# Optimization experiments

Hardware: AMD Instinct MI355X
Metric: run time of the kernel (lower is better)

The kernel has to match this reference:

```python
import jax, jax.numpy as jnp
import numpy as np

N, D_IN, D_HID, D_OUT, ORDER = 8192, 512, 1024, 64, 3

def setup_inputs() -> dict:
    key = jax.random.key(0)
    k = jax.random.split(key, 5)
    x = jax.random.normal(k[0], (N, D_IN), dtype=jnp.float32)
    adj = jax.random.uniform(k[1], (ORDER, N, N), dtype=jnp.float32)
    W1 = jax.random.normal(k[2], (ORDER, D_IN, D_HID), dtype=jnp.float32) * (1.0 / np.sqrt(D_IN))
    b1 = jnp.zeros((D_HID,), dtype=jnp.float32)
    W2 = jax.random.normal(k[3], (ORDER, D_HID, D_OUT), dtype=jnp.float32) * (1.0 / np.sqrt(D_HID))
    b2 = jnp.zeros((D_OUT,), dtype=jnp.float32)
    return {"x": x, "preprocessed": adj, "W1": W1, "b1": b1, "W2": W2, "b2": b2}

def multi_val_gc(x, adj, W, b):
    # x: [N, in], adj: [order, N, N], W: [order, in, out]
    xw = jnp.einsum('ni,kio->kno', x, W)          # [order, N, out]
    out = jnp.einsum('knm,kmo->no', adj, xw)      # sum over orders
    return out + b

def reference(x, preprocessed, W1, b1, W2, b2):
    h = multi_val_gc(x, preprocessed, W1, b1)
    h = jax.nn.relu(h)
    # dropout is identity in eval mode
    h = multi_val_gc(h, preprocessed, W2, b2)
    return jax.nn.log_softmax(h, axis=1)
```

## Files before the change

### kernel.cpp

```cpp
#include <hip/hip_runtime.h>
#include <hip/hip_bf16.h>
#include <cstdint>
#include <cstddef>


typedef __bf16 bf16_t;
typedef __bf16 bf16x8 __attribute__((ext_vector_type(8)));
typedef __bf16 bf16x4 __attribute__((ext_vector_type(4)));
typedef float  f32x4  __attribute__((ext_vector_type(4)));

#define NROWS 8192
#define DIN   512
#define DHID  1024
#define DOUT  64
#define ORD   3
#define KTOT  24576

#define GLDS(g, l) __builtin_amdgcn_global_load_lds( \
    (__attribute__((address_space(1))) void*)(g),    \
    (__attribute__((address_space(3))) void*)(l), 16, 0, 0)


__global__ void k_cvt_x(const float* __restrict__ x, bf16_t* __restrict__ xb) {
  int i = blockIdx.x * blockDim.x + threadIdx.x;
  const float4* p = reinterpret_cast<const float4*>(x) + (size_t)i * 2;
  float4 v0 = p[0], v1 = p[1];
  bf16x8 o;
  o[0]=(bf16_t)v0.x; o[1]=(bf16_t)v0.y; o[2]=(bf16_t)v0.z; o[3]=(bf16_t)v0.w;
  o[4]=(bf16_t)v1.x; o[5]=(bf16_t)v1.y; o[6]=(bf16_t)v1.z; o[7]=(bf16_t)v1.w;
  *reinterpret_cast<bf16x8*>(xb + (size_t)i * 8) = o;
}

__global__ void k_cvt_adj(const float* __restrict__ a, bf16_t* __restrict__ ab) {
  size_t i = (size_t)blockIdx.x * blockDim.x + threadIdx.x;
  const size_t stride = (size_t)gridDim.x * blockDim.x;
  const float4* src = reinterpret_cast<const float4*>(a);
#pragma unroll 4
  for (int it = 0; it < 48; ++it, i += stride) {
    float4 v0 = src[i * 2], v1 = src[i * 2 + 1];
    bf16x8 o;
    o[0]=(bf16_t)v0.x; o[1]=(bf16_t)v0.y; o[2]=(bf16_t)v0.z; o[3]=(bf16_t)v0.w;
    o[4]=(bf16_t)v1.x; o[5]=(bf16_t)v1.y; o[6]=(bf16_t)v1.z; o[7]=(bf16_t)v1.w;
    *reinterpret_cast<bf16x8*>(ab + i * 8) = o;
  }
}

__global__ void k_transpose_cvt(const float* __restrict__ src, bf16_t* __restrict__ dst,
                                int R, int C) {
  __shared__ float tile[64][65];
  int ord = blockIdx.z;
  src += (size_t)ord * R * C;
  dst += (size_t)ord * R * C;
  int c0 = blockIdx.x * 64, r0 = blockIdx.y * 64;
  for (int i = 0; i < 16; ++i) {
    int idx = i * 256 + threadIdx.x;
    int r = idx >> 6, c = idx & 63;
    tile[r][c] = src[(size_t)(r0 + r) * C + c0 + c];
  }
  __syncthreads();
  for (int i = 0; i < 16; ++i) {
    int idx = i * 256 + threadIdx.x;
    int cc = idx >> 6, rr = idx & 63;
    dst[(size_t)(c0 + cc) * R + r0 + rr] = (bf16_t)tile[rr][cc];
  }
}

__global__ __launch_bounds__(256) void k_gemm_xw1(
    const bf16_t* __restrict__ xb,
    const bf16_t* __restrict__ w1t,
    bf16_t* __restrict__ xw1t)
{
  __shared__ bf16_t As[128 * 64];
  __shared__ bf16_t Bs[128 * 64];
  int ntile = blockIdx.x, mtile = blockIdx.y, ord = blockIdx.z;
  int tid = threadIdx.x, lane = tid & 63, wid = tid >> 6;
  int wm = wid >> 1, wn = wid & 1;
  int sl = (lane & 7) ^ (lane >> 3);
  f32x4 acc[4][4] = {};
  const bf16_t* w1o = w1t + (size_t)ord * DHID * DIN;
  for (int kt = 0; kt < DIN; kt += 64) {
    for (int j = 0; j < 4; ++j) {
      int q = wid * 4 + j;
      int row = q * 8 + (lane >> 3);
      GLDS(xb + (size_t)(mtile * 128 + row) * DIN + kt + sl * 8, &As[q * 512]);
    }
    for (int j = 0; j < 4; ++j) {
      int q = wid * 4 + j;
      int row = q * 8 + (lane >> 3);
      GLDS(w1o + (size_t)(ntile * 128 + row) * DIN + kt + sl * 8, &Bs[q * 512]);
    }
    __syncthreads();
    for (int ks = 0; ks < 2; ++ks) {
      int psl = ((ks << 2) + (lane >> 4)) ^ (lane & 7);
      bf16x8 a[4], b[4];
      for (int f = 0; f < 4; ++f)
        a[f] = *reinterpret_cast<const bf16x8*>(&As[(wm * 64 + f * 16 + (lane & 15)) * 64 + psl * 8]);
      for (int f = 0; f < 4; ++f)
        b[f] = *reinterpret_cast<const bf16x8*>(&Bs[(wn * 64 + f * 16 + (lane & 15)) * 64 + psl * 8]);
      for (int fm = 0; fm < 4; ++fm)
        for (int fn = 0; fn < 4; ++fn)
          acc[fm][fn] = __builtin_amdgcn_mfma_f32_16x16x32_bf16(a[fm], b[fn], acc[fm][fn], 0, 0, 0);
    }
    __syncthreads();
  }
  for (int fm = 0; fm < 4; ++fm)
    for (int fn = 0; fn < 4; ++fn) {
      int o  = ntile * 128 + wn * 64 + fn * 16 + (lane & 15);
      int n0 = mtile * 128 + wm * 64 + fm * 16 + ((lane >> 4) << 2);
      bf16x4 v;
      v[0] = (bf16_t)acc[fm][fn][0]; v[1] = (bf16_t)acc[fm][fn][1];
      v[2] = (bf16_t)acc[fm][fn][2]; v[3] = (bf16_t)acc[fm][fn][3];
      *reinterpret_cast<bf16x4*>(&xw1t[(size_t)o * KTOT + ord * NROWS + n0]) = v;
    }
}

__global__ __launch_bounds__(512) void k_gemm_h256(
    const bf16_t* __restrict__ adjb,
    const bf16_t* __restrict__ xw1t,
    float* __restrict__ hpart)
{
  __shared__ bf16_t As[256 * 64];
  __shared__ bf16_t Bs[256 * 64];
  int d = blockIdx.x;
  int xcd = d & 7;
  int s = d >> 3;
  int ksp = xcd & 1;
  int mtile = (xcd >> 1) * 8 + (s >> 2);
  int ntile = s & 3;
  int tid = threadIdx.x, lane = tid & 63, wid = tid >> 6;
  int wm = wid >> 2, wn = wid & 3;
  int sl = (lane & 7) ^ (lane >> 3);
  const size_t NN = (size_t)NROWS * NROWS;
  f32x4 acc[8][4] = {};
  const int T0 = ksp * 192, NT = 192;

  for (int t = 0; t < NT; ++t) {
    int kk = (T0 + t) * 64;
    int ord = kk >> 13, mcol = kk & 8191;
    const bf16_t* ao = adjb + (size_t)ord * NN + (size_t)(mtile * 256) * NROWS + mcol;
#pragma unroll
    for (int j = 0; j < 4; ++j) {
      int q = wid * 4 + j;
      int row = q * 8 + (lane >> 3);
      GLDS(ao + (size_t)row * NROWS + sl * 8, &As[q * 512]);
    }
#pragma unroll
    for (int j = 0; j < 4; ++j) {
      int q = wid * 4 + j;
      int row = q * 8 + (lane >> 3);
      GLDS(xw1t + (size_t)(ntile * 256 + row) * KTOT + kk + sl * 8, &Bs[q * 512]);
    }
    __syncthreads();
#pragma unroll
    for (int ks = 0; ks < 2; ++ks) {
      int psl = ((ks << 2) + (lane >> 4)) ^ (lane & 7);
      bf16x8 a[8], b[4];
#pragma unroll
      for (int f = 0; f < 8; ++f)
        a[f] = *reinterpret_cast<const bf16x8*>(&As[(wm * 128 + f * 16 + (lane & 15)) * 64 + psl * 8]);
#pragma unroll
      for (int f = 0; f < 4; ++f)
        b[f] = *reinterpret_cast<const bf16x8*>(&Bs[(wn * 64 + f * 16 + (lane & 15)) * 64 + psl * 8]);
#pragma unroll
      for (int fm = 0; fm < 8; ++fm)
#pragma unroll
        for (int fn = 0; fn < 4; ++fn)
          acc[fm][fn] = __builtin_amdgcn_mfma_f32_16x16x32_bf16(a[fm], b[fn], acc[fm][fn], 0, 0, 0);
    }
    __syncthreads();
  }

  float* pout = hpart + (size_t)ksp * NROWS * DHID;
#pragma unroll
  for (int fm = 0; fm < 8; ++fm)
#pragma unroll
    for (int fn = 0; fn < 4; ++fn) {
      int o  = ntile * 256 + wn * 64 + fn * 16 + (lane & 15);
      int n0 = mtile * 256 + wm * 128 + fm * 16 + ((lane >> 4) << 2);
      for (int j = 0; j < 4; ++j)
        pout[(size_t)(n0 + j) * DHID + o] = acc[fm][fn][j];
    }
}

__global__ void k_reduce_h(const float* __restrict__ hpart, const float* __restrict__ b1,
                           bf16_t* __restrict__ h) {
  size_t i4 = (size_t)blockIdx.x * blockDim.x + threadIdx.x;
  size_t base = i4 * 4;
  int col = (int)(base & (DHID - 1));
  const size_t S = (size_t)NROWS * DHID;
  float4 p0 = *reinterpret_cast<const float4*>(hpart + base);
  float4 p1 = *reinterpret_cast<const float4*>(hpart + S + base);
  float4 bb = *reinterpret_cast<const float4*>(b1 + col);
  bf16x4 v;
  float t0 = p0.x + p1.x + bb.x; v[0] = (bf16_t)(t0 > 0.f ? t0 : 0.f);
  float t1 = p0.y + p1.y + bb.y; v[1] = (bf16_t)(t1 > 0.f ? t1 : 0.f);
  float t2 = p0.z + p1.z + bb.z; v[2] = (bf16_t)(t2 > 0.f ? t2 : 0.f);
  float t3 = p0.w + p1.w + bb.w; v[3] = (bf16_t)(t3 > 0.f ? t3 : 0.f);
  *reinterpret_cast<bf16x4*>(h + base) = v;
}

__global__ __launch_bounds__(256) void k_gemm_h128(
    const bf16_t* __restrict__ adjb, const bf16_t* __restrict__ xw1t,
    const float* __restrict__ b1, bf16_t* __restrict__ h)
{
  __shared__ bf16_t As[2][128 * 64];
  __shared__ bf16_t Bs[2][128 * 64];
  int d = blockIdx.x;
  int xcd = d & 7;
  int idx = d >> 3;
  int mtile = xcd * 8 + (idx >> 3);
  int ntile = idx & 7;
  int tid = threadIdx.x, lane = tid & 63, wid = tid >> 6;
  int wm = wid >> 1, wn = wid & 1;
  int sl = (lane & 7) ^ (lane >> 3);
  const size_t NN = (size_t)NROWS * NROWS;
  f32x4 acc[4][4] = {};
  const int NT = KTOT / 64;

  auto stage = [&](int buf, int kt) {
    int kk = kt * 64;
    int ord = kk >> 13, mcol = kk & 8191;
    const bf16_t* ao = adjb + (size_t)ord * NN + (size_t)(mtile * 128) * NROWS + mcol;
#pragma unroll
    for (int jj = 0; jj < 4; ++jj) {
      int q = wid * 4 + jj;
      int row = q * 8 + (lane >> 3);
      GLDS(ao + (size_t)row * NROWS + sl * 8, &As[buf][q * 512]);
    }
#pragma unroll
    for (int jj = 0; jj < 4; ++jj) {
      int q = wid * 4 + jj;
      int row = q * 8 + (lane >> 3);
      GLDS(xw1t + (size_t)(ntile * 128 + row) * KTOT + kk + sl * 8, &Bs[buf][q * 512]);
    }
  };
  auto compute = [&](int cur) {
    const bf16_t* Ac = &As[cur][0];
    const bf16_t* Bc = &Bs[cur][0];
#pragma unroll
    for (int ks = 0; ks < 2; ++ks) {
      int psl = ((ks << 2) + (lane >> 4)) ^ (lane & 7);
      bf16x8 a[4], b[4];
      for (int f = 0; f < 4; ++f)
        a[f] = *reinterpret_cast<const bf16x8*>(&Ac[(wm * 64 + f * 16 + (lane & 15)) * 64 + psl * 8]);
      for (int f = 0; f < 4; ++f)
        b[f] = *reinterpret_cast<const bf16x8*>(&Bc[(wn * 64 + f * 16 + (lane & 15)) * 64 + psl * 8]);
      for (int fm = 0; fm < 4; ++fm)
        for (int fn = 0; fn < 4; ++fn)
          acc[fm][fn] = __builtin_amdgcn_mfma_f32_16x16x32_bf16(a[fm], b[fn], acc[fm][fn], 0, 0, 0);
    }
  };

  stage(0, 0);
  for (int t = 0; t < NT - 1; ++t) {
    int cur = t & 1;
    stage(cur ^ 1, t + 1);
    asm volatile("s_waitcnt vmcnt(8)" ::: "memory");
    __builtin_amdgcn_s_barrier();
    compute(cur);
    asm volatile("" ::: "memory");
    __builtin_amdgcn_s_barrier();
  }
  asm volatile("s_waitcnt vmcnt(0)" ::: "memory");
  __builtin_amdgcn_s_barrier();
  compute((NT - 1) & 1);

  for (int fm = 0; fm < 4; ++fm)
    for (int fn = 0; fn < 4; ++fn) {
      int o  = ntile * 128 + wn * 64 + fn * 16 + (lane & 15);
      float bias = b1[o];
      int n0 = mtile * 128 + wm * 64 + fm * 16 + ((lane >> 4) << 2);
      for (int jj = 0; jj < 4; ++jj) {
        float v = acc[fm][fn][jj] + bias;
        v = v > 0.0f ? v : 0.0f;
        h[(size_t)(n0 + jj) * DHID + o] = (bf16_t)v;
      }
    }
}

__global__ __launch_bounds__(256) void k_gemm_xw2(
    const bf16_t* __restrict__ h,
    const bf16_t* __restrict__ w2t,
    bf16_t* __restrict__ xw2t)
{
  __shared__ bf16_t As[128 * 64];
  __shared__ bf16_t Bs[64 * 64];
  int mtile = blockIdx.x, ord = blockIdx.y;
  int tid = threadIdx.x, lane = tid & 63, wid = tid >> 6;
  int wm = wid >> 1, wn = wid & 1;
  int sl = (lane & 7) ^ (lane >> 3);
  f32x4 acc[4][2] = {};
  const bf16_t* w2o = w2t + (size_t)ord * DOUT * DHID;
  for (int kt = 0; kt < DHID; kt += 64) {
    for (int j = 0; j < 4; ++j) {
      int q = wid * 4 + j;
      int row = q * 8 + (lane >> 3);
      GLDS(h + (size_t)(mtile * 128 + row) * DHID + kt + sl * 8, &As[q * 512]);
    }
    for (int j = 0; j < 2; ++j) {
      int q = wid * 2 + j;
      int row = q * 8 + (lane >> 3);
      GLDS(w2o + (size_t)row * DHID + kt + sl * 8, &Bs[q * 512]);
    }
    __syncthreads();
    for (int ks = 0; ks < 2; ++ks) {
      int psl = ((ks << 2) + (lane >> 4)) ^ (lane & 7);
      bf16x8 a[4], b[2];
      for (int f = 0; f < 4; ++f)
        a[f] = *reinterpret_cast<const bf16x8*>(&As[(wm * 64 + f * 16 + (lane & 15)) * 64 + psl * 8]);
      for (int f = 0; f < 2; ++f)
        b[f] = *reinterpret_cast<const bf16x8*>(&Bs[(wn * 32 + f * 16 + (lane & 15)) * 64 + psl * 8]);
      for (int fm = 0; fm < 4; ++fm)
        for (int fn = 0; fn < 2; ++fn)
          acc[fm][fn] = __builtin_amdgcn_mfma_f32_16x16x32_bf16(a[fm], b[fn], acc[fm][fn], 0, 0, 0);
    }
    __syncthreads();
  }
  for (int fm = 0; fm < 4; ++fm)
    for (int fn = 0; fn < 2; ++fn) {
      int o2 = wn * 32 + fn * 16 + (lane & 15);
      int n0 = mtile * 128 + wm * 64 + fm * 16 + ((lane >> 4) << 2);
      bf16x4 v;
      v[0] = (bf16_t)acc[fm][fn][0]; v[1] = (bf16_t)acc[fm][fn][1];
      v[2] = (bf16_t)acc[fm][fn][2]; v[3] = (bf16_t)acc[fm][fn][3];
      *reinterpret_cast<bf16x4*>(&xw2t[(size_t)o2 * KTOT + ord * NROWS + n0]) = v;
    }
}

__global__ __launch_bounds__(256) void k_gemm_out(
    const bf16_t* __restrict__ adjb,
    const bf16_t* __restrict__ xw2t,
    float* __restrict__ part)
{
  __shared__ bf16_t As[128 * 64];
  __shared__ bf16_t Bs[64 * 64];
  int mtile = blockIdx.x, ksp = blockIdx.y;
  int tid = threadIdx.x, lane = tid & 63, wid = tid >> 6;
  int wm = wid >> 1, wn = wid & 1;
  int sl = (lane & 7) ^ (lane >> 3);
  const size_t NN = (size_t)NROWS * NROWS;
  f32x4 acc[4][2] = {};
  for (int kt = ksp * 24; kt < ksp * 24 + 24; ++kt) {
    int kk = kt * 64;
    int ord = kk >> 13, mcol = kk & 8191;
    const bf16_t* ao = adjb + (size_t)ord * NN + (size_t)(mtile * 128) * NROWS + mcol;
    for (int j = 0; j < 4; ++j) {
      int q = wid * 4 + j;
      int row = q * 8 + (lane >> 3);
      GLDS(ao + (size_t)row * NROWS + sl * 8, &As[q * 512]);
    }
    for (int j = 0; j < 2; ++j) {
      int q = wid * 2 + j;
      int row = q * 8 + (lane >> 3);
      GLDS(xw2t + (size_t)row * KTOT + kk + sl * 8, &Bs[q * 512]);
    }
    __syncthreads();
    for (int ks = 0; ks < 2; ++ks) {
      int psl = ((ks << 2) + (lane >> 4)) ^ (lane & 7);
      bf16x8 a[4], b[2];
      for (int f = 0; f < 4; ++f)
        a[f] = *reinterpret_cast<const bf16x8*>(&As[(wm * 64 + f * 16 + (lane & 15)) * 64 + psl * 8]);
      for (int f = 0; f < 2; ++f)
        b[f] = *reinterpret_cast<const bf16x8*>(&Bs[(wn * 32 + f * 16 + (lane & 15)) * 64 + psl * 8]);
      for (int fm = 0; fm < 4; ++fm)
        for (int fn = 0; fn < 2; ++fn)
          acc[fm][fn] = __builtin_amdgcn_mfma_f32_16x16x32_bf16(a[fm], b[fn], acc[fm][fn], 0, 0, 0);
    }
    __syncthreads();
  }
  float* pout = part + (size_t)ksp * NROWS * DOUT;
  for (int fm = 0; fm < 4; ++fm)
    for (int fn = 0; fn < 2; ++fn) {
      int o2 = wn * 32 + fn * 16 + (lane & 15);
      int n0 = mtile * 128 + wm * 64 + fm * 16 + ((lane >> 4) << 2);
      for (int j = 0; j < 4; ++j)
        pout[(size_t)(n0 + j) * DOUT + o2] = acc[fm][fn][j];
    }
}

__global__ void k_logsoftmax(const float* __restrict__ part, const float* __restrict__ b2,
                             float* __restrict__ out) {
  int wid = threadIdx.x >> 6, lane = threadIdx.x & 63;
  int n = blockIdx.x * 4 + wid;
  size_t s = (size_t)NROWS * DOUT;
  float v = b2[lane];
#pragma unroll
  for (int p = 0; p < 16; ++p)
    v += part[(size_t)p * s + (size_t)n * DOUT + lane];
  float mx = v;
  for (int d = 32; d; d >>= 1) mx = fmaxf(mx, __shfl_xor(mx, d));
  float e = expf(v - mx);
  float sum = e;
  for (int d = 32; d; d >>= 1) sum += __shfl_xor(sum, d);
  out[(size_t)n * DOUT + lane] = (v - mx) - logf(sum);
}

__global__ __launch_bounds__(256) void k_gemm_h_f32(
    const float* __restrict__ adj, const bf16_t* __restrict__ xw1t,
    const float* __restrict__ b1, bf16_t* __restrict__ h)
{
  __shared__ bf16_t As[128 * 64];
  __shared__ bf16_t Bs[128 * 64];
  int d = blockIdx.x;
  int xcd = d & 7, idx = d >> 3;
  int mtile = xcd * 8 + (idx >> 3), ntile = idx & 7;
  int tid = threadIdx.x, lane = tid & 63, wid = tid >> 6;
  int wm = wid >> 1, wn = wid & 1;
  int sl = (lane & 7) ^ (lane >> 3);
  f32x4 acc[4][4] = {};
  for (int kt = 0; kt < KTOT / 64; ++kt) {
    int kk0 = kt * 64;
    int ord = kk0 >> 13, mcol = kk0 & 8191;
    for (int j = 0; j < 4; ++j) {
      int q = wid * 4 + j;
      int row = q * 8 + (lane >> 3);
      GLDS(xw1t + (size_t)(ntile * 128 + row) * KTOT + kk0 + sl * 8, &Bs[q * 512]);
    }
    const float* abase = adj + (size_t)ord * NROWS * NROWS + (size_t)(mtile * 128) * NROWS + mcol;
    bf16x8 st[4]; int mrow[4], kb[4];
    for (int i = 0; i < 4; ++i) {
      int c = i * 256 + tid;
      mrow[i] = c >> 3; kb[i] = c & 7;
      const float4* p = reinterpret_cast<const float4*>(abase + (size_t)mrow[i] * NROWS + kb[i] * 8);
      float4 v0 = p[0], v1 = p[1];
      bf16x8 o;
      o[0]=(bf16_t)v0.x; o[1]=(bf16_t)v0.y; o[2]=(bf16_t)v0.z; o[3]=(bf16_t)v0.w;
      o[4]=(bf16_t)v1.x; o[5]=(bf16_t)v1.y; o[6]=(bf16_t)v1.z; o[7]=(bf16_t)v1.w;
      st[i] = o;
    }
    for (int i = 0; i < 4; ++i)
      *reinterpret_cast<bf16x8*>(&As[mrow[i] * 64 + (kb[i] ^ (mrow[i] & 7)) * 8]) = st[i];
    __syncthreads();
    for (int ks = 0; ks < 2; ++ks) {
      int psl = ((ks << 2) + (lane >> 4)) ^ (lane & 7);
      bf16x8 a[4], b[4];
      for (int f = 0; f < 4; ++f)
        a[f] = *reinterpret_cast<const bf16x8*>(&As[(wm * 64 + f * 16 + (lane & 15)) * 64 + psl * 8]);
      for (int f = 0; f < 4; ++f)
        b[f] = *reinterpret_cast<const bf16x8*>(&Bs[(wn * 64 + f * 16 + (lane & 15)) * 64 + psl * 8]);
      for (int fm = 0; fm < 4; ++fm)
        for (int fn = 0; fn < 4; ++fn)
          acc[fm][fn] = __builtin_amdgcn_mfma_f32_16x16x32_bf16(a[fm], b[fn], acc[fm][fn], 0, 0, 0);
    }
    __syncthreads();
  }
  for (int fm = 0; fm < 4; ++fm)
    for (int fn = 0; fn < 4; ++fn) {
      int o  = ntile * 128 + wn * 64 + fn * 16 + (lane & 15);
      float bias = b1[o];
      int n0 = mtile * 128 + wm * 64 + fm * 16 + ((lane >> 4) << 2);
      for (int j = 0; j < 4; ++j) {
        float v = acc[fm][fn][j] + bias;
        v = v > 0.0f ? v : 0.0f;
        h[(size_t)(n0 + j) * DHID + o] = (bf16_t)v;
      }
    }
}

__global__ __launch_bounds__(256) void k_gemm_out_f32(
    const float* __restrict__ adj, const bf16_t* __restrict__ xw2t,
    float* __restrict__ part)
{
  __shared__ bf16_t As[128 * 64];
  __shared__ bf16_t Bs[64 * 64];
  int mtile = blockIdx.x, ksp = blockIdx.y;
  int tid = threadIdx.x, lane = tid & 63, wid = tid >> 6;
  int wm = wid >> 1, wn = wid & 1;
  int sl = (lane & 7) ^ (lane >> 3);
  f32x4 acc[4][2] = {};
  for (int kt = ksp * 24; kt < ksp * 24 + 24; ++kt) {
    int kk0 = kt * 64;
    int ord = kk0 >> 13, mcol = kk0 & 8191;
    for (int j = 0; j < 2; ++j) {
      int q = wid * 2 + j;
      int row = q * 8 + (lane >> 3);
      GLDS(xw2t + (size_t)row * KTOT + kk0 + sl * 8, &Bs[q * 512]);
    }
    const float* abase = adj + (size_t)ord * NROWS * NROWS + (size_t)(mtile * 128) * NROWS + mcol;
    bf16x8 st[4]; int mrow[4], kb[4];
    for (int i = 0; i < 4; ++i) {
      int c = i * 256 + tid;
      mrow[i] = c >> 3; kb[i] = c & 7;
      const float4* p = reinterpret_cast<const float4*>(abase + (size_t)mrow[i] * NROWS + kb[i] * 8);
      float4 v0 = p[0], v1 = p[1];
      bf16x8 o;
      o[0]=(bf16_t)v0.x; o[1]=(bf16_t)v0.y; o[2]=(bf16_t)v0.z; o[3]=(bf16_t)v0.w;
      o[4]=(bf16_t)v1.x; o[5]=(bf16_t)v1.y; o[6]=(bf16_t)v1.z; o[7]=(bf16_t)v1.w;
      st[i] = o;
    }
    for (int i = 0; i < 4; ++i)
      *reinterpret_cast<bf16x8*>(&As[mrow[i] * 64 + (kb[i] ^ (mrow[i] & 7)) * 8]) = st[i];
    __syncthreads();
    for (int ks = 0; ks < 2; ++ks) {
      int psl = ((ks << 2) + (lane >> 4)) ^ (lane & 7);
      bf16x8 a[4], b[2];
      for (int f = 0; f < 4; ++f)
        a[f] = *reinterpret_cast<const bf16x8*>(&As[(wm * 64 + f * 16 + (lane & 15)) * 64 + psl * 8]);
      for (int f = 0; f < 2; ++f)
        b[f] = *reinterpret_cast<const bf16x8*>(&Bs[(wn * 32 + f * 16 + (lane & 15)) * 64 + psl * 8]);
      for (int fm = 0; fm < 4; ++fm)
        for (int fn = 0; fn < 2; ++fn)
          acc[fm][fn] = __builtin_amdgcn_mfma_f32_16x16x32_bf16(a[fm], b[fn], acc[fm][fn], 0, 0, 0);
    }
    __syncthreads();
  }
  float* pout = part + (size_t)ksp * NROWS * DOUT;
  for (int fm = 0; fm < 4; ++fm)
    for (int fn = 0; fn < 2; ++fn) {
      int o2 = wn * 32 + fn * 16 + (lane & 15);
      int n0 = mtile * 128 + wm * 64 + fm * 16 + ((lane >> 4) << 2);
      for (int j = 0; j < 4; ++j)
        pout[(size_t)(n0 + j) * DOUT + o2] = acc[fm][fn][j];
    }
}

extern "C" void kernel_launch(void* const* d_in, const int* in_sizes, int n_in,
                              void* d_out, int out_size, void* d_ws, size_t ws_size,
                              hipStream_t stream) {
  const float* x   = (const float*)d_in[0];
  const float* adj = (const float*)d_in[1];
  const float* W1  = (const float*)d_in[2];
  const float* b1  = (const float*)d_in[3];
  const float* W2  = (const float*)d_in[4];
  const float* b2  = (const float*)d_in[5];
  float* out = (float*)d_out;
  char* ws = (char*)d_ws;

  const size_t ADJB_SZ  = 402653184ULL;
  const size_t NEED_OLD = 484835328ULL;
  const size_t NEED_NEW = 551944192ULL;

  if (ws_size >= NEED_OLD) {
    bf16_t* adjb = (bf16_t*)(ws + 0);
    bf16_t* xb   = (bf16_t*)(ws + ADJB_SZ);
    bf16_t* w1t  = (bf16_t*)(ws + ADJB_SZ + 8388608);
    bf16_t* w2t  = (bf16_t*)(ws + ADJB_SZ + 11534336);
    bf16_t* xw1t = (bf16_t*)(ws + ADJB_SZ + 11927552);
    bf16_t* h    = (bf16_t*)(ws + ADJB_SZ + 62259200);
    bf16_t* xw2t = (bf16_t*)(ws + ADJB_SZ + 79036416);
    float*  hpart = (float*)(ws + ADJB_SZ + 82182144);
    float*  part = (ws_size >= NEED_NEW) ? hpart
                                         : (float*)(ws + ADJB_SZ + 11927552);

    k_cvt_adj<<<2048, 256, 0, stream>>>(adj, adjb);
    k_cvt_x<<<2048, 256, 0, stream>>>(x, xb);
    k_transpose_cvt<<<dim3(16, 8, 3), 256, 0, stream>>>(W1, w1t, DIN, DHID);
    k_transpose_cvt<<<dim3(1, 16, 3), 256, 0, stream>>>(W2, w2t, DHID, DOUT);
    k_gemm_xw1<<<dim3(8, 64, 3), 256, 0, stream>>>(xb, w1t, xw1t);
    if (ws_size >= NEED_NEW) {
      k_gemm_h256<<<256, 512, 0, stream>>>(adjb, xw1t, hpart);
      k_reduce_h<<<8192, 256, 0, stream>>>(hpart, b1, h);
    } else {
      k_gemm_h128<<<512, 256, 0, stream>>>(adjb, xw1t, b1, h);
    }
    k_gemm_xw2<<<dim3(64, 3), 256, 0, stream>>>(h, w2t, xw2t);
    k_gemm_out<<<dim3(64, 16), 256, 0, stream>>>(adjb, xw2t, part);
    k_logsoftmax<<<2048, 256, 0, stream>>>(part, b2, out);
  } else {
    bf16_t* xb   = (bf16_t*)(ws + 0);
    bf16_t* w1t  = (bf16_t*)(ws + 8388608);
    bf16_t* w2t  = (bf16_t*)(ws + 11534336);
    bf16_t* xw1t = (bf16_t*)(ws + 11927552);
    bf16_t* h    = (bf16_t*)(ws + 62259200);
    bf16_t* xw2t = (bf16_t*)(ws + 79036416);
    float*  part = (float*)(ws + 11927552);

    k_cvt_x<<<2048, 256, 0, stream>>>(x, xb);
    k_transpose_cvt<<<dim3(16, 8, 3), 256, 0, stream>>>(W1, w1t, DIN, DHID);
    k_transpose_cvt<<<dim3(1, 16, 3), 256, 0, stream>>>(W2, w2t, DHID, DOUT);
    k_gemm_xw1<<<dim3(8, 64, 3), 256, 0, stream>>>(xb, w1t, xw1t);
    k_gemm_h_f32<<<512, 256, 0, stream>>>(adj, xw1t, b1, h);
    k_gemm_xw2<<<dim3(64, 3), 256, 0, stream>>>(h, w2t, xw2t);
    k_gemm_out_f32<<<dim3(64, 16), 256, 0, stream>>>(adj, xw2t, part);
    k_logsoftmax<<<2048, 256, 0, stream>>>(part, b2, out);
  }
}
```

Measured before the change: 950.1 us.

## Double-buffer LDS tiles in the big adjacency GEMM to overlap loads with MFMA

Splits the A and B LDS tiles of the main adjacency×XW GEMM into two buffers and prefetches the next k-tile with global_load_lds while computing on the current one. Each thread waits only for the older batch of loads (vmcnt(8)) before the barrier. This is meant to hide global memory latency behind the MFMA work. LDS use doubles to 128KB per block, which may limit occupancy, and the reliance on vmcnt ordering plus raw barriers carries a correctness risk.

```diff
diff --git a/kernel.cpp b/kernel.cpp
--- a/kernel.cpp
+++ b/kernel.cpp
@@ -119,8 +119,8 @@
     const bf16_t* __restrict__ xw1t,
     float* __restrict__ hpart)
 {
-  __shared__ bf16_t As[256 * 64];
-  __shared__ bf16_t Bs[256 * 64];
+  __shared__ bf16_t As[2][256 * 64];
+  __shared__ bf16_t Bs[2][256 * 64];
   int d = blockIdx.x;
   int xcd = d & 7;
   int s = d >> 3;
@@ -134,7 +134,7 @@
   f32x4 acc[8][4] = {};
   const int T0 = ksp * 192, NT = 192;
 
-  for (int t = 0; t < NT; ++t) {
+  auto stage = [&](int buf, int t) {
     int kk = (T0 + t) * 64;
     int ord = kk >> 13, mcol = kk & 8191;
     const bf16_t* ao = adjb + (size_t)ord * NN + (size_t)(mtile * 256) * NROWS + mcol;
@@ -142,33 +142,50 @@
     for (int j = 0; j < 4; ++j) {
       int q = wid * 4 + j;
       int row = q * 8 + (lane >> 3);
-      GLDS(ao + (size_t)row * NROWS + sl * 8, &As[q * 512]);
-    }
-#pragma unroll
-    for (int j = 0; j < 4; ++j) {
-      int q = wid * 4 + j;
-      int row = q * 8 + (lane >> 3);
-      GLDS(xw1t + (size_t)(ntile * 256 + row) * KTOT + kk + sl * 8, &Bs[q * 512]);
-    }
-    __syncthreads();
+      GLDS(ao + (size_t)row * NROWS + sl * 8, &As[buf][q * 512]);
+    }
+#pragma unroll
+    for (int j = 0; j < 4; ++j) {
+      int q = wid * 4 + j;
+      int row = q * 8 + (lane >> 3);
+      GLDS(xw1t + (size_t)(ntile * 256 + row) * KTOT + kk + sl * 8, &Bs[buf][q * 512]);
+    }
+  };
+
+  auto compute = [&](int cur) {
+    const bf16_t* Ac = &As[cur][0];
+    const bf16_t* Bc = &Bs[cur][0];
 #pragma unroll
     for (int ks = 0; ks < 2; ++ks) {
       int psl = ((ks << 2) + (lane >> 4)) ^ (lane & 7);
       bf16x8 a[8], b[4];
 #pragma unroll
       for (int f = 0; f < 8; ++f)
-        a[f] = *reinterpret_cast<const bf16x8*>(&As[(wm * 128 + f * 16 + (lane & 15)) * 64 + psl * 8]);
-#pragma unroll
-      for (int f = 0; f < 4; ++f)
-        b[f] = *reinterpret_cast<const bf16x8*>(&Bs[(wn * 64 + f * 16 + (lane & 15)) * 64 + psl * 8]);
+        a[f] = *reinterpret_cast<const bf16x8*>(&Ac[(wm * 128 + f * 16 + (lane & 15)) * 64 + psl * 8]);
+#pragma unroll
+      for (int f = 0; f < 4; ++f)
+        b[f] = *reinterpret_cast<const bf16x8*>(&Bc[(wn * 64 + f * 16 + (lane & 15)) * 64 + psl * 8]);
 #pragma unroll
       for (int fm = 0; fm < 8; ++fm)
 #pragma unroll
         for (int fn = 0; fn < 4; ++fn)
           acc[fm][fn] = __builtin_amdgcn_mfma_f32_16x16x32_bf16(a[fm], b[fn], acc[fm][fn], 0, 0, 0);
     }
-    __syncthreads();
-  }
+  };
+
+  stage(0, 0);
+  for (int t = 0; t < NT - 1; ++t) {
+    int cur = t & 1;
+    stage(cur ^ 1, t + 1);
+    asm volatile("s_waitcnt vmcnt(8)" ::: "memory");
+    __builtin_amdgcn_s_barrier();
+    compute(cur);
+    asm volatile("" ::: "memory");
+    __builtin_amdgcn_s_barrier();
+  }
+  asm volatile("s_waitcnt vmcnt(0)" ::: "memory");
+  __builtin_amdgcn_s_barrier();
+  compute((NT - 1) & 1);
 
   float* pout = hpart + (size_t)ksp * NROWS * DHID;
 #pragma unroll
```

After: 889.4 us, median of 2. 1.07x faster.
